# Kernel optimization log

Hardware: AMD Instinct MI355X
Metric: run time of the kernel (lower is better)

## Reference

```python
import jax, jax.numpy as jnp
import numpy as np

FIN, FOUT, BATCH = 1024, 1024, 256


def setup_inputs() -> dict:
    key = jax.random.key(0)
    k1, k2, k3, k4 = jax.random.split(key, 4)
    x = jax.random.normal(k1, (BATCH, FIN), dtype=jnp.float32)
    m = jax.random.uniform(k2, (BATCH, FOUT, FIN), dtype=jnp.float32)
    weight = jax.random.normal(k3, (FOUT, FIN), dtype=jnp.float32) * (1.0 / np.sqrt(FIN))
    bias = jax.random.normal(k4, (FOUT,), dtype=jnp.float32) * 0.01
    return {"x": x, "m": m, "weight": weight, "bias": bias}


def reference(x, m, weight, bias):
    # Fused equivalent of: (weight * m).permute(0,2,1) then einsum('ac,acb->ab', x, .) + bias
    # out[b,o] = sum_f x[b,f] * weight[o,f] * m[b,o,f] + bias[o]
    out = jnp.einsum('bf,of,bof->bo', x, weight, m) + bias
    return out
```

## Files before the change

### kernel.cpp

```cpp
#include <hip/hip_runtime.h>


#define FIN   1024
#define FOUT  1024
#define BATCH 256

__global__ __launch_bounds__(256) void dwa_row_reduce(
    const float* __restrict__ x,
    const float* __restrict__ m,
    const float* __restrict__ w,
    const float* __restrict__ bias,
    float* __restrict__ out)
{
    const int gtid = blockIdx.x * blockDim.x + threadIdx.x;
    const int wave = gtid >> 6;
    const int lane = threadIdx.x & 63;

    const int b = wave >> 10;
    const int o = wave & (FOUT - 1);

    const float* mrow = m + ((size_t)b * FOUT + (size_t)o) * FIN;
    const float* xrow = x + (size_t)b * FIN;
    const float* wrow = w + (size_t)o * FIN;

    float acc = 0.0f;
#pragma unroll
    for (int c = 0; c < FIN / (64 * 4); ++c) {
        const int f = c * 256 + lane * 4;
        const float4 mv = *reinterpret_cast<const float4*>(mrow + f);
        const float4 xv = *reinterpret_cast<const float4*>(xrow + f);
        const float4 wv = *reinterpret_cast<const float4*>(wrow + f);
        acc += mv.x * xv.x * wv.x;
        acc += mv.y * xv.y * wv.y;
        acc += mv.z * xv.z * wv.z;
        acc += mv.w * xv.w * wv.w;
    }

#pragma unroll
    for (int off = 32; off > 0; off >>= 1)
        acc += __shfl_down(acc, off, 64);

    if (lane == 0)
        out[(size_t)b * FOUT + o] = acc + bias[o];
}

extern "C" void kernel_launch(void* const* d_in, const int* in_sizes, int n_in,
                              void* d_out, int out_size, void* d_ws, size_t ws_size,
                              hipStream_t stream) {
    const float* x    = (const float*)d_in[0];
    const float* m    = (const float*)d_in[1];
    const float* wgt  = (const float*)d_in[2];
    const float* bias = (const float*)d_in[3];
    float* out = (float*)d_out;

    const int total_waves   = BATCH * FOUT;
    const int threads       = 256;
    const int waves_per_blk = threads / 64;
    const int blocks        = total_waves / waves_per_blk;

    dwa_row_reduce<<<blocks, threads, 0, stream>>>(x, m, wgt, bias, out);
}
```

Baseline: 217.5 us.

## Process 32 rows per wave with cached x and nontemporal m loads

After: 206.7 us. -4.9%, faster.

```diff
diff --git a/kernel.cpp b/kernel.cpp
--- a/kernel.cpp
+++ b/kernel.cpp
@@ -4,6 +4,9 @@
 #define FIN   1024
 #define FOUT  1024
 #define BATCH 256
+#define ROWS_PER_WAVE 32
+
+typedef float v4f __attribute__((ext_vector_type(4)));
 
 __global__ __launch_bounds__(256) void dwa_row_reduce(
     const float* __restrict__ x,
@@ -16,32 +19,45 @@
     const int wave = gtid >> 6;
     const int lane = threadIdx.x & 63;
 
-    const int b = wave >> 10;
-    const int o = wave & (FOUT - 1);
+    const int row0 = wave * ROWS_PER_WAVE;
+    const int b    = row0 >> 10;
+    const int o0   = row0 & (FOUT - 1);
 
-    const float* mrow = m + ((size_t)b * FOUT + (size_t)o) * FIN;
-    const float* xrow = x + (size_t)b * FIN;
-    const float* wrow = w + (size_t)o * FIN;
-
-    float acc = 0.0f;
+    v4f xv[4];
+    {
+        const float* xrow = x + (size_t)b * FIN;
 #pragma unroll
-    for (int c = 0; c < FIN / (64 * 4); ++c) {
-        const int f = c * 256 + lane * 4;
-        const float4 mv = *reinterpret_cast<const float4*>(mrow + f);
-        const float4 xv = *reinterpret_cast<const float4*>(xrow + f);
-        const float4 wv = *reinterpret_cast<const float4*>(wrow + f);
-        acc += mv.x * xv.x * wv.x;
-        acc += mv.y * xv.y * wv.y;
-        acc += mv.z * xv.z * wv.z;
-        acc += mv.w * xv.w * wv.w;
+        for (int c = 0; c < 4; ++c)
+            xv[c] = *reinterpret_cast<const v4f*>(xrow + c * 256 + lane * 4);
     }
 
+    const float* mrow = m + (size_t)row0 * FIN;
+    const float* wrow = w + (size_t)o0 * FIN;
+
+#pragma unroll 2
+    for (int r = 0; r < ROWS_PER_WAVE; ++r) {
+        float acc = 0.0f;
 #pragma unroll
-    for (int off = 32; off > 0; off >>= 1)
-        acc += __shfl_down(acc, off, 64);
+        for (int c = 0; c < 4; ++c) {
+            const int f = c * 256 + lane * 4;
+            const v4f mv = __builtin_nontemporal_load(
+                                reinterpret_cast<const v4f*>(mrow + f));
+            const v4f wv = *reinterpret_cast<const v4f*>(wrow + f);
+            acc += xv[c].x * wv.x * mv.x;
+            acc += xv[c].y * wv.y * mv.y;
+            acc += xv[c].z * wv.z * mv.z;
+            acc += xv[c].w * wv.w * mv.w;
+        }
+#pragma unroll
+        for (int off = 32; off > 0; off >>= 1)
+            acc += __shfl_down(acc, off, 64);
 
-    if (lane == 0)
-        out[(size_t)b * FOUT + o] = acc + bias[o];
+        if (lane == 0)
+            out[row0 + r] = acc + bias[o0 + r];
+
+        mrow += FIN;
+        wrow += FIN;
+    }
 }
 
 extern "C" void kernel_launch(void* const* d_in, const int* in_sizes, int n_in,
@@ -53,10 +69,10 @@
     const float* bias = (const float*)d_in[3];
     float* out = (float*)d_out;
 
-    const int total_waves   = BATCH * FOUT;
-    const int threads       = 256;
-    const int waves_per_blk = threads / 64;
-    const int blocks        = total_waves / waves_per_blk;
+    const int total_rows = BATCH * FOUT;
+    const int waves      = total_rows / ROWS_PER_WAVE;
+    const int threads    = 256;
+    const int blocks     = waves / (threads / 64);
 
     dwa_row_reduce<<<blocks, threads, 0, stream>>>(x, m, wgt, bias, out);
 }
```
